# Performance work log

Measured on AMD Instinct MI355X. Metric: run time of the kernel, lower is better.

The kernel has to match this reference:

```python
import jax, jax.numpy as jnp
import numpy as np

N_NODES = 50000


def gcn_conv(x, W, b, src, dst, n):
    """PyG-style GCNConv: symmetric-normalized aggregation over A + I.
    x: [N, Fin], W: [Fin, Fout], b: [Fout], src/dst: [E] int edge endpoints.
    """
    h = x @ W  # [N, Fout]
    # degree with self-loops: deg[i] = 1 + in-degree(i)
    deg = jnp.zeros((n,), dtype=h.dtype).at[dst].add(1.0) + 1.0
    dinv = jax.lax.rsqrt(deg)  # deg^-1/2
    norm_e = dinv[src] * dinv[dst]  # [E]
    # message passing: sum_j norm_ij * h_j  (plus self-loop term deg_i^-1 * h_i)
    agg = jnp.zeros_like(h).at[dst].add(h[src] * norm_e[:, None])
    agg = agg + h * (dinv * dinv)[:, None]
    return agg + b


def setup_inputs() -> dict:
    key = jax.random.key(0)
    ks = jax.random.split(key, 9)
    N, F_in, H, C = N_NODES, 128, 64, 4
    E = 1600000
    node_features = jax.random.normal(ks[0], (N, F_in), dtype=jnp.float32)
    edge_index = jax.random.randint(ks[1], (2, E), 0, N, dtype=jnp.int32)
    s1 = 1.0 / np.sqrt(F_in)
    s2 = 1.0 / np.sqrt(H)
    W1 = jax.random.uniform(ks[2], (F_in, H), jnp.float32, -s1, s1)
    b1 = jax.random.uniform(ks[3], (H,), jnp.float32, -s1, s1)
    W2 = jax.random.uniform(ks[4], (H, H), jnp.float32, -s2, s2)
    b2 = jax.random.uniform(ks[5], (H,), jnp.float32, -s2, s2)
    W3 = jax.random.uniform(ks[6], (H, C), jnp.float32, -s2, s2)
    b3 = jax.random.uniform(ks[7], (C,), jnp.float32, -s2, s2)
    return {"node_features": node_features, "edge_index": edge_index,
            "W1": W1, "b1": b1, "W2": W2, "b2": b2, "W3": W3, "b3": b3}


def reference(node_features, edge_index, W1, b1, W2, b2, W3, b3):
    n = node_features.shape[0]
    src, dst = edge_index[0], edge_index[1]
    out = jax.nn.relu(gcn_conv(node_features, W1, b1, src, dst, n))
    # layer2 applied 7 times with SHARED weights (faithful to the source)
    for _ in range(7):
        out = jax.nn.relu(gcn_conv(out, W2, b2, src, dst, n))
    out = gcn_conv(out, W3, b3, src, dst, n)
    return jax.nn.softmax(out, axis=0)  # softmax over the node dimension (dim=0)
```

## Files before the change

kernel.cpp:

```cpp
#include <hip/hip_runtime.h>
#include <hip/hip_fp16.h>
#include <math.h>
#include <float.h>


#define NPART 8
#define BPP   104


__global__ __launch_bounds__(256) void k_count(const int* __restrict__ dst,
                                               unsigned* __restrict__ deg,
                                               int E, int chunk) {
    int part = blockIdx.x & (NPART - 1);
    int q = blockIdx.x >> 3;
    int lo = part * chunk, hi = lo + chunk;
    for (int e = q * 256 + threadIdx.x; e < E; e += 256 * BPP) {
        int d = dst[e];
        if (d >= lo && d < hi) atomicAdd(&deg[d], 1u);
    }
}

__global__ __launch_bounds__(256) void k_dinv(const unsigned* __restrict__ deg,
                                              float* __restrict__ dinv, int n) {
    int i = blockIdx.x * 256 + threadIdx.x;
    if (i < n) dinv[i] = rsqrtf(1.0f + (float)deg[i]);
}

__global__ __launch_bounds__(256) void k_scan1(const unsigned* __restrict__ deg,
                                               int* __restrict__ row_start,
                                               unsigned* __restrict__ bsum, int n) {
    __shared__ unsigned t[256];
    int i = blockIdx.x * 256 + threadIdx.x;
    unsigned v = (i < n) ? deg[i] : 0u;
    t[threadIdx.x] = v;
    __syncthreads();
    #pragma unroll
    for (int off = 1; off < 256; off <<= 1) {
        unsigned u = (threadIdx.x >= (unsigned)off) ? t[threadIdx.x - off] : 0u;
        __syncthreads();
        t[threadIdx.x] += u;
        __syncthreads();
    }
    if (i < n) row_start[i] = (int)(t[threadIdx.x] - v);
    if (threadIdx.x == 255) bsum[blockIdx.x] = t[255];
}

__global__ __launch_bounds__(256) void k_scan2(unsigned* __restrict__ bsum,
                                               int* __restrict__ row_start,
                                               int nb, int n) {
    __shared__ unsigned t[256];
    unsigned v = (threadIdx.x < (unsigned)nb) ? bsum[threadIdx.x] : 0u;
    t[threadIdx.x] = v;
    __syncthreads();
    #pragma unroll
    for (int off = 1; off < 256; off <<= 1) {
        unsigned u = (threadIdx.x >= (unsigned)off) ? t[threadIdx.x - off] : 0u;
        __syncthreads();
        t[threadIdx.x] += u;
        __syncthreads();
    }
    if (threadIdx.x < (unsigned)nb) bsum[threadIdx.x] = t[threadIdx.x] - v;
    if (threadIdx.x == 255) row_start[n] = (int)t[255];
}

__global__ __launch_bounds__(256) void k_scan3(int* __restrict__ row_start,
                                               const unsigned* __restrict__ bsum, int n) {
    int i = blockIdx.x * 256 + threadIdx.x;
    if (i < n) row_start[i] += (int)bsum[blockIdx.x];
}

__global__ __launch_bounds__(256) void k_fill(const int* __restrict__ src,
                                              const int* __restrict__ dst,
                                              const int* __restrict__ row_start,
                                              unsigned* __restrict__ cursor,
                                              int* __restrict__ csr_src,
                                              int E, int chunk) {
    int part = blockIdx.x & (NPART - 1);
    int q = blockIdx.x >> 3;
    int lo = part * chunk, hi = lo + chunk;
    for (int e = q * 256 + threadIdx.x; e < E; e += 256 * BPP) {
        int d = dst[e];
        if (d >= lo && d < hi) {
            int s = src[e];
            unsigned pos = atomicAdd(&cursor[d], 1u);
            csr_src[row_start[d] + (int)pos] = s;
        }
    }
}


__global__ __launch_bounds__(256) void k_gemm64_f32(const float* __restrict__ x,
                                                    const float* __restrict__ W,
                                                    const float* __restrict__ dinv,
                                                    __half* __restrict__ hs, int n) {
    __shared__ float Wl[128 * 64];
    for (int idx = threadIdx.x; idx < 128 * 64; idx += 256) Wl[idx] = W[idx];
    __syncthreads();
    int wave = threadIdx.x >> 6, lane = threadIdx.x & 63;
    int base = blockIdx.x * 64 + wave * 16;
    for (int it = 0; it < 16; ++it) {
        int i = base + it;
        if (i < n) {
            const float4* xr = (const float4*)(x + (size_t)i * 128);
            float acc = 0.f;
            #pragma unroll
            for (int k4 = 0; k4 < 32; ++k4) {
                float4 v = xr[k4];
                acc += v.x * Wl[(k4 * 4 + 0) * 64 + lane];
                acc += v.y * Wl[(k4 * 4 + 1) * 64 + lane];
                acc += v.z * Wl[(k4 * 4 + 2) * 64 + lane];
                acc += v.w * Wl[(k4 * 4 + 3) * 64 + lane];
            }
            hs[(size_t)i * 64 + lane] = __float2half(acc * dinv[i]);
        }
    }
}


__global__ __launch_bounds__(256) void k_gemm64_f16(const __half* __restrict__ xh,
                                                    const float* __restrict__ W,
                                                    const float* __restrict__ dinv,
                                                    __half* __restrict__ hs, int n) {
    __shared__ float Wl[64 * 64];
    for (int idx = threadIdx.x; idx < 64 * 64; idx += 256) Wl[idx] = W[idx];
    __syncthreads();
    int wave = threadIdx.x >> 6, lane = threadIdx.x & 63;
    int base = blockIdx.x * 64 + wave * 16;
    for (int it = 0; it < 16; ++it) {
        int i = base + it;
        if (i < n) {
            const __half2* xr = (const __half2*)(xh + (size_t)i * 64);
            float acc = 0.f;
            #pragma unroll
            for (int k2 = 0; k2 < 32; ++k2) {
                float2 v = __half22float2(xr[k2]);
                acc += v.x * Wl[(k2 * 2 + 0) * 64 + lane];
                acc += v.y * Wl[(k2 * 2 + 1) * 64 + lane];
            }
            hs[(size_t)i * 64 + lane] = __float2half(acc * dinv[i]);
        }
    }
}

__global__ __launch_bounds__(256) void k_gemm4(const __half* __restrict__ xh,
                                               const float* __restrict__ W,
                                               const float* __restrict__ dinv,
                                               float4* __restrict__ h4, int n) {
    __shared__ float Wl[256];
    for (int idx = threadIdx.x; idx < 256; idx += 256) Wl[idx] = W[idx];
    __syncthreads();
    int i = blockIdx.x * 256 + threadIdx.x;
    if (i >= n) return;
    const __half2* ar = (const __half2*)(xh + (size_t)i * 64);
    float a0 = 0.f, a1 = 0.f, a2 = 0.f, a3 = 0.f;
    #pragma unroll
    for (int k2 = 0; k2 < 32; ++k2) {
        float2 v = __half22float2(ar[k2]);
        int k = k2 * 2;
        a0 += v.x * Wl[k * 4 + 0] + v.y * Wl[(k + 1) * 4 + 0];
        a1 += v.x * Wl[k * 4 + 1] + v.y * Wl[(k + 1) * 4 + 1];
        a2 += v.x * Wl[k * 4 + 2] + v.y * Wl[(k + 1) * 4 + 2];
        a3 += v.x * Wl[k * 4 + 3] + v.y * Wl[(k + 1) * 4 + 3];
    }
    float di = dinv[i];
    h4[i] = make_float4(a0 * di, a1 * di, a2 * di, a3 * di);
}


__global__ __launch_bounds__(256) void k_agg64h(const __half* __restrict__ hs,
                                                const float* __restrict__ dinv,
                                                const int* __restrict__ row_start,
                                                const int* __restrict__ csr_src,
                                                const float* __restrict__ bias,
                                                __half* __restrict__ out, int n) {
    int gw = (int)((blockIdx.x * 256 + threadIdx.x) >> 6);
    int lane = threadIdx.x & 63;
    if (gw >= n) return;
    float acc = __half2float(hs[(size_t)gw * 64 + lane]);
    int s = row_start[gw], e = row_start[gw + 1];
    int slot = s;
    for (; slot + 16 <= e; slot += 16) {
        int idx[16];
        #pragma unroll
        for (int j = 0; j < 16; ++j) idx[j] = csr_src[slot + j];
        float v[16];
        #pragma unroll
        for (int j = 0; j < 16; ++j) v[j] = __half2float(hs[(size_t)idx[j] * 64 + lane]);
        float t0 = ((v[0] + v[1]) + (v[2] + v[3])) + ((v[4] + v[5]) + (v[6] + v[7]));
        float t1 = ((v[8] + v[9]) + (v[10] + v[11])) + ((v[12] + v[13]) + (v[14] + v[15]));
        acc += t0 + t1;
    }
    for (; slot + 4 <= e; slot += 4) {
        int i0 = csr_src[slot + 0], i1 = csr_src[slot + 1];
        int i2 = csr_src[slot + 2], i3 = csr_src[slot + 3];
        float v0 = __half2float(hs[(size_t)i0 * 64 + lane]);
        float v1 = __half2float(hs[(size_t)i1 * 64 + lane]);
        float v2 = __half2float(hs[(size_t)i2 * 64 + lane]);
        float v3 = __half2float(hs[(size_t)i3 * 64 + lane]);
        acc += (v0 + v1) + (v2 + v3);
    }
    for (; slot < e; ++slot)
        acc += __half2float(hs[(size_t)csr_src[slot] * 64 + lane]);
    acc = acc * dinv[gw] + bias[lane];
    out[(size_t)gw * 64 + lane] = __float2half(fmaxf(acc, 0.f));
}


__global__ __launch_bounds__(256) void k_agg4(const float4* __restrict__ h4,
                                              const float* __restrict__ dinv,
                                              const int* __restrict__ row_start,
                                              const int* __restrict__ csr_src,
                                              const float* __restrict__ b3,
                                              float4* __restrict__ z, int n) {
    int i = blockIdx.x * 256 + threadIdx.x;
    if (i >= n) return;
    float4 self = h4[i];
    float a0 = self.x, a1 = self.y, a2 = self.z, a3 = self.w;
    int s = row_start[i], e = row_start[i + 1];
    int slot = s;
    for (; slot + 4 <= e; slot += 4) {
        int s0 = csr_src[slot], s1 = csr_src[slot + 1];
        int s2 = csr_src[slot + 2], s3 = csr_src[slot + 3];
        float4 v0 = h4[s0], v1 = h4[s1], v2 = h4[s2], v3 = h4[s3];
        a0 += v0.x + v1.x + v2.x + v3.x;
        a1 += v0.y + v1.y + v2.y + v3.y;
        a2 += v0.z + v1.z + v2.z + v3.z;
        a3 += v0.w + v1.w + v2.w + v3.w;
    }
    for (; slot < e; ++slot) {
        float4 v = h4[csr_src[slot]];
        a0 += v.x; a1 += v.y; a2 += v.z; a3 += v.w;
    }
    float di = dinv[i];
    z[i] = make_float4(a0 * di + b3[0], a1 * di + b3[1],
                       a2 * di + b3[2], a3 * di + b3[3]);
}


__device__ inline unsigned encf(float f) {
    unsigned u = __float_as_uint(f);
    return (u & 0x80000000u) ? ~u : (u | 0x80000000u);
}
__device__ inline float decf(unsigned e) {
    return (e & 0x80000000u) ? __uint_as_float(e & 0x7FFFFFFFu) : __uint_as_float(~e);
}

__global__ __launch_bounds__(256) void k_max(const float4* __restrict__ z,
                                             unsigned* __restrict__ gmax, int n) {
    float m0 = -FLT_MAX, m1 = -FLT_MAX, m2 = -FLT_MAX, m3 = -FLT_MAX;
    for (int i = blockIdx.x * 256 + threadIdx.x; i < n; i += gridDim.x * 256) {
        float4 v = z[i];
        m0 = fmaxf(m0, v.x); m1 = fmaxf(m1, v.y);
        m2 = fmaxf(m2, v.z); m3 = fmaxf(m3, v.w);
    }
    #pragma unroll
    for (int off = 32; off; off >>= 1) {
        m0 = fmaxf(m0, __shfl_xor(m0, off));
        m1 = fmaxf(m1, __shfl_xor(m1, off));
        m2 = fmaxf(m2, __shfl_xor(m2, off));
        m3 = fmaxf(m3, __shfl_xor(m3, off));
    }
    if ((threadIdx.x & 63) == 0) {
        atomicMax(&gmax[0], encf(m0));
        atomicMax(&gmax[1], encf(m1));
        atomicMax(&gmax[2], encf(m2));
        atomicMax(&gmax[3], encf(m3));
    }
}

__global__ __launch_bounds__(256) void k_exp(const float4* __restrict__ z,
                                             float4* __restrict__ out,
                                             const unsigned* __restrict__ gmax,
                                             float* __restrict__ gsum, int n) {
    float M0 = decf(gmax[0]), M1 = decf(gmax[1]), M2 = decf(gmax[2]), M3 = decf(gmax[3]);
    float s0 = 0.f, s1 = 0.f, s2 = 0.f, s3 = 0.f;
    for (int i = blockIdx.x * 256 + threadIdx.x; i < n; i += gridDim.x * 256) {
        float4 v = z[i];
        float4 e;
        e.x = expf(v.x - M0); e.y = expf(v.y - M1);
        e.z = expf(v.z - M2); e.w = expf(v.w - M3);
        out[i] = e;
        s0 += e.x; s1 += e.y; s2 += e.z; s3 += e.w;
    }
    #pragma unroll
    for (int off = 32; off; off >>= 1) {
        s0 += __shfl_xor(s0, off);
        s1 += __shfl_xor(s1, off);
        s2 += __shfl_xor(s2, off);
        s3 += __shfl_xor(s3, off);
    }
    if ((threadIdx.x & 63) == 0) {
        atomicAdd(&gsum[0], s0);
        atomicAdd(&gsum[1], s1);
        atomicAdd(&gsum[2], s2);
        atomicAdd(&gsum[3], s3);
    }
}

__global__ __launch_bounds__(256) void k_norm(float4* __restrict__ out,
                                              const float* __restrict__ gsum, int n) {
    float r0 = 1.f / gsum[0], r1 = 1.f / gsum[1], r2 = 1.f / gsum[2], r3 = 1.f / gsum[3];
    for (int i = blockIdx.x * 256 + threadIdx.x; i < n; i += gridDim.x * 256) {
        float4 v = out[i];
        v.x *= r0; v.y *= r1; v.z *= r2; v.w *= r3;
        out[i] = v;
    }
}


extern "C" void kernel_launch(void* const* d_in, const int* in_sizes, int n_in,
                              void* d_out, int out_size, void* d_ws, size_t ws_size,
                              hipStream_t stream) {
    const float* x0 = (const float*)d_in[0];
    const int* ei = (const int*)d_in[1];
    const float* W1 = (const float*)d_in[2];
    const float* b1 = (const float*)d_in[3];
    const float* W2 = (const float*)d_in[4];
    const float* b2 = (const float*)d_in[5];
    const float* W3 = (const float*)d_in[6];
    const float* b3 = (const float*)d_in[7];

    const int n = in_sizes[0] / 128;
    const int E = in_sizes[1] / 2;
    const int* src = ei;
    const int* dst = ei + E;
    const int chunk = (n + NPART - 1) / NPART;

    char* ws = (char*)d_ws;
    size_t off = 0;
    auto alloc = [&](size_t bytes) -> void* {
        void* p = (void*)(ws + off);
        off = (off + bytes + 255) & ~(size_t)255;
        return p;
    };

    unsigned* deg    = (unsigned*)alloc((size_t)n * 4);
    unsigned* cursor = (unsigned*)alloc((size_t)n * 4);
    unsigned* gmax   = (unsigned*)alloc(16);
    float*    gsum   = (float*)alloc(16);
    size_t zero_bytes = off;

    float* dinv      = (float*)alloc((size_t)n * 4);
    int*   row_start = (int*)alloc((size_t)(n + 1) * 4);
    unsigned* bsum   = (unsigned*)alloc(1024 * 4);
    int*   csr_src   = (int*)alloc((size_t)E * 4);
    __half* hbuf     = (__half*)alloc((size_t)n * 64 * 2);
    __half* xbuf     = (__half*)alloc((size_t)n * 64 * 2);
    float4* h4buf    = (float4*)alloc((size_t)n * 16);
    float4* zbuf     = (float4*)alloc((size_t)n * 16);

    hipMemsetAsync(deg, 0, zero_bytes, stream);

    const int nbN = (n + 255) / 256;

    k_count<<<NPART * BPP, 256, 0, stream>>>(dst, deg, E, chunk);
    k_dinv<<<nbN, 256, 0, stream>>>(deg, dinv, n);
    k_scan1<<<nbN, 256, 0, stream>>>(deg, row_start, bsum, n);
    k_scan2<<<1, 256, 0, stream>>>(bsum, row_start, nbN, n);
    k_scan3<<<nbN, 256, 0, stream>>>(row_start, bsum, n);
    k_fill<<<NPART * BPP, 256, 0, stream>>>(src, dst, row_start, cursor, csr_src, E, chunk);

    const int nbG = (n + 63) / 64;
    const int nbA = (n * 64 + 255) / 256;

    k_gemm64_f32<<<nbG, 256, 0, stream>>>(x0, W1, dinv, hbuf, n);
    k_agg64h<<<nbA, 256, 0, stream>>>(hbuf, dinv, row_start, csr_src, b1, xbuf, n);

    for (int l = 0; l < 7; ++l) {
        k_gemm64_f16<<<nbG, 256, 0, stream>>>(xbuf, W2, dinv, hbuf, n);
        k_agg64h<<<nbA, 256, 0, stream>>>(hbuf, dinv, row_start, csr_src, b2, xbuf, n);
    }

    k_gemm4<<<nbN, 256, 0, stream>>>(xbuf, W3, dinv, h4buf, n);
    k_agg4<<<nbN, 256, 0, stream>>>(h4buf, dinv, row_start, csr_src, b3, zbuf, n);

    k_max<<<256, 256, 0, stream>>>(zbuf, gmax, n);
    k_exp<<<256, 256, 0, stream>>>(zbuf, (float4*)d_out, gmax, gsum, n);
    k_norm<<<256, 256, 0, stream>>>((float4*)d_out, gsum, n);
}
```

Baseline: 899.4 us.

## Register-block GEMMs over four rows per wave and add nontemporal streaming loads

The dense GEMM kernels now have each wave compute four rows at once. Each shared-memory weight read is reused across four accumulators, and the grid is enlarged so each block handles 16 rows instead of 64. Weight staging into LDS is vectorized with float4. Nontemporal load hints are applied to streamed edge/CSR index reads and GEMM input rows to reduce cache pollution, at the risk of hurting reuse of csr_src across the repeated aggregation layers.

```diff
diff --git a/kernel.cpp b/kernel.cpp
--- a/kernel.cpp
+++ b/kernel.cpp
@@ -6,6 +6,8 @@
 
 #define NPART 8
 #define BPP   104
+
+typedef float f4 __attribute__((ext_vector_type(4)));
 
 
 __global__ __launch_bounds__(256) void k_count(const int* __restrict__ dst,
@@ -15,7 +17,7 @@
     int q = blockIdx.x >> 3;
     int lo = part * chunk, hi = lo + chunk;
     for (int e = q * 256 + threadIdx.x; e < E; e += 256 * BPP) {
-        int d = dst[e];
+        int d = __builtin_nontemporal_load(&dst[e]);
         if (d >= lo && d < hi) atomicAdd(&deg[d], 1u);
     }
 }
@@ -79,9 +81,9 @@
     int q = blockIdx.x >> 3;
     int lo = part * chunk, hi = lo + chunk;
     for (int e = q * 256 + threadIdx.x; e < E; e += 256 * BPP) {
-        int d = dst[e];
+        int d = __builtin_nontemporal_load(&dst[e]);
         if (d >= lo && d < hi) {
-            int s = src[e];
+            int s = __builtin_nontemporal_load(&src[e]);
             unsigned pos = atomicAdd(&cursor[d], 1u);
             csr_src[row_start[d] + (int)pos] = s;
         }
@@ -94,18 +96,47 @@
                                                     const float* __restrict__ dinv,
                                                     __half* __restrict__ hs, int n) {
     __shared__ float Wl[128 * 64];
-    for (int idx = threadIdx.x; idx < 128 * 64; idx += 256) Wl[idx] = W[idx];
+    {
+        const f4* Wv = (const f4*)W;
+        f4* Wlv = (f4*)Wl;
+        for (int idx = threadIdx.x; idx < 128 * 16; idx += 256) Wlv[idx] = Wv[idx];
+    }
     __syncthreads();
     int wave = threadIdx.x >> 6, lane = threadIdx.x & 63;
-    int base = blockIdx.x * 64 + wave * 16;
-    for (int it = 0; it < 16; ++it) {
-        int i = base + it;
-        if (i < n) {
-            const float4* xr = (const float4*)(x + (size_t)i * 128);
+    int i0 = blockIdx.x * 16 + wave * 4;
+    if (i0 >= n) return;
+    if (i0 + 3 < n) {
+        const f4* r0 = (const f4*)(x + (size_t)(i0 + 0) * 128);
+        const f4* r1 = (const f4*)(x + (size_t)(i0 + 1) * 128);
+        const f4* r2 = (const f4*)(x + (size_t)(i0 + 2) * 128);
+        const f4* r3 = (const f4*)(x + (size_t)(i0 + 3) * 128);
+        float a0 = 0.f, a1 = 0.f, a2 = 0.f, a3 = 0.f;
+        #pragma unroll
+        for (int k4 = 0; k4 < 32; ++k4) {
+            f4 v0 = __builtin_nontemporal_load(&r0[k4]);
+            f4 v1 = __builtin_nontemporal_load(&r1[k4]);
+            f4 v2 = __builtin_nontemporal_load(&r2[k4]);
+            f4 v3 = __builtin_nontemporal_load(&r3[k4]);
+            float w0 = Wl[(k4 * 4 + 0) * 64 + lane];
+            float w1 = Wl[(k4 * 4 + 1) * 64 + lane];
+            float w2 = Wl[(k4 * 4 + 2) * 64 + lane];
+            float w3 = Wl[(k4 * 4 + 3) * 64 + lane];
+            a0 += v0.x * w0 + v0.y * w1 + v0.z * w2 + v0.w * w3;
+            a1 += v1.x * w0 + v1.y * w1 + v1.z * w2 + v1.w * w3;
+            a2 += v2.x * w0 + v2.y * w1 + v2.z * w2 + v2.w * w3;
+            a3 += v3.x * w0 + v3.y * w1 + v3.z * w2 + v3.w * w3;
+        }
+        hs[(size_t)(i0 + 0) * 64 + lane] = __float2half(a0 * dinv[i0 + 0]);
+        hs[(size_t)(i0 + 1) * 64 + lane] = __float2half(a1 * dinv[i0 + 1]);
+        hs[(size_t)(i0 + 2) * 64 + lane] = __float2half(a2 * dinv[i0 + 2]);
+        hs[(size_t)(i0 + 3) * 64 + lane] = __float2half(a3 * dinv[i0 + 3]);
+    } else {
+        for (int i = i0; i < n && i < i0 + 4; ++i) {
+            const f4* r = (const f4*)(x + (size_t)i * 128);
             float acc = 0.f;
             #pragma unroll
             for (int k4 = 0; k4 < 32; ++k4) {
-                float4 v = xr[k4];
+                f4 v = r[k4];
                 acc += v.x * Wl[(k4 * 4 + 0) * 64 + lane];
                 acc += v.y * Wl[(k4 * 4 + 1) * 64 + lane];
                 acc += v.z * Wl[(k4 * 4 + 2) * 64 + lane];
@@ -122,18 +153,49 @@
                                                     const float* __restrict__ dinv,
                                                     __half* __restrict__ hs, int n) {
     __shared__ float Wl[64 * 64];
-    for (int idx = threadIdx.x; idx < 64 * 64; idx += 256) Wl[idx] = W[idx];
+    {
+        const f4* Wv = (const f4*)W;
+        f4* Wlv = (f4*)Wl;
+        for (int idx = threadIdx.x; idx < 64 * 16; idx += 256) Wlv[idx] = Wv[idx];
+    }
     __syncthreads();
     int wave = threadIdx.x >> 6, lane = threadIdx.x & 63;
-    int base = blockIdx.x * 64 + wave * 16;
-    for (int it = 0; it < 16; ++it) {
-        int i = base + it;
-        if (i < n) {
-            const __half2* xr = (const __half2*)(xh + (size_t)i * 64);
+    int i0 = blockIdx.x * 16 + wave * 4;
+    if (i0 >= n) return;
+    if (i0 + 3 < n) {
+        const unsigned* r0 = (const unsigned*)(xh + (size_t)(i0 + 0) * 64);
+        const unsigned* r1 = (const unsigned*)(xh + (size_t)(i0 + 1) * 64);
+        const unsigned* r2 = (const unsigned*)(xh + (size_t)(i0 + 2) * 64);
+        const unsigned* r3 = (const unsigned*)(xh + (size_t)(i0 + 3) * 64);
+        float a0 = 0.f, a1 = 0.f, a2 = 0.f, a3 = 0.f;
+        #pragma unroll
+        for (int k2 = 0; k2 < 32; ++k2) {
+            unsigned u0 = __builtin_nontemporal_load(&r0[k2]);
+            unsigned u1 = __builtin_nontemporal_load(&r1[k2]);
+            unsigned u2 = __builtin_nontemporal_load(&r2[k2]);
+            unsigned u3 = __builtin_nontemporal_load(&r3[k2]);
+            float w0 = Wl[(k2 * 2 + 0) * 64 + lane];
+            float w1 = Wl[(k2 * 2 + 1) * 64 + lane];
+            float2 v0 = __half22float2(*(__half2*)&u0);
+            float2 v1 = __half22float2(*(__half2*)&u1);
+            float2 v2 = __half22float2(*(__half2*)&u2);
+            float2 v3 = __half22float2(*(__half2*)&u3);
+            a0 += v0.x * w0 + v0.y * w1;
+            a1 += v1.x * w0 + v1.y * w1;
+            a2 += v2.x * w0 + v2.y * w1;
+            a3 += v3.x * w0 + v3.y * w1;
+        }
+        hs[(size_t)(i0 + 0) * 64 + lane] = __float2half(a0 * dinv[i0 + 0]);
+        hs[(size_t)(i0 + 1) * 64 + lane] = __float2half(a1 * dinv[i0 + 1]);
+        hs[(size_t)(i0 + 2) * 64 + lane] = __float2half(a2 * dinv[i0 + 2]);
+        hs[(size_t)(i0 + 3) * 64 + lane] = __float2half(a3 * dinv[i0 + 3]);
+    } else {
+        for (int i = i0; i < n && i < i0 + 4; ++i) {
+            const __half2* r = (const __half2*)(xh + (size_t)i * 64);
             float acc = 0.f;
             #pragma unroll
             for (int k2 = 0; k2 < 32; ++k2) {
-                float2 v = __half22float2(xr[k2]);
+                float2 v = __half22float2(r[k2]);
                 acc += v.x * Wl[(k2 * 2 + 0) * 64 + lane];
                 acc += v.y * Wl[(k2 * 2 + 1) * 64 + lane];
             }
@@ -182,7 +244,7 @@
     for (; slot + 16 <= e; slot += 16) {
         int idx[16];
         #pragma unroll
-        for (int j = 0; j < 16; ++j) idx[j] = csr_src[slot + j];
+        for (int j = 0; j < 16; ++j) idx[j] = __builtin_nontemporal_load(&csr_src[slot + j]);
         float v[16];
         #pragma unroll
         for (int j = 0; j < 16; ++j) v[j] = __half2float(hs[(size_t)idx[j] * 64 + lane]);
@@ -191,8 +253,10 @@
         acc += t0 + t1;
     }
     for (; slot + 4 <= e; slot += 4) {
-        int i0 = csr_src[slot + 0], i1 = csr_src[slot + 1];
-        int i2 = csr_src[slot + 2], i3 = csr_src[slot + 3];
+        int i0 = __builtin_nontemporal_load(&csr_src[slot + 0]);
+        int i1 = __builtin_nontemporal_load(&csr_src[slot + 1]);
+        int i2 = __builtin_nontemporal_load(&csr_src[slot + 2]);
+        int i3 = __builtin_nontemporal_load(&csr_src[slot + 3]);
         float v0 = __half2float(hs[(size_t)i0 * 64 + lane]);
         float v1 = __half2float(hs[(size_t)i1 * 64 + lane]);
         float v2 = __half2float(hs[(size_t)i2 * 64 + lane]);
@@ -219,8 +283,10 @@
     int s = row_start[i], e = row_start[i + 1];
     int slot = s;
     for (; slot + 4 <= e; slot += 4) {
-        int s0 = csr_src[slot], s1 = csr_src[slot + 1];
-        int s2 = csr_src[slot + 2], s3 = csr_src[slot + 3];
+        int s0 = __builtin_nontemporal_load(&csr_src[slot + 0]);
+        int s1 = __builtin_nontemporal_load(&csr_src[slot + 1]);
+        int s2 = __builtin_nontemporal_load(&csr_src[slot + 2]);
+        int s3 = __builtin_nontemporal_load(&csr_src[slot + 3]);
         float4 v0 = h4[s0], v1 = h4[s1], v2 = h4[s2], v3 = h4[s3];
         a0 += v0.x + v1.x + v2.x + v3.x;
         a1 += v0.y + v1.y + v2.y + v3.y;
@@ -360,7 +426,7 @@
     k_scan3<<<nbN, 256, 0, stream>>>(row_start, bsum, n);
     k_fill<<<NPART * BPP, 256, 0, stream>>>(src, dst, row_start, cursor, csr_src, E, chunk);
 
-    const int nbG = (n + 63) / 64;
+    const int nbG = (n + 15) / 16;
     const int nbA = (n * 64 + 255) / 256;
 
     k_gemm64_f32<<<nbG, 256, 0, stream>>>(x0, W1, dinv, hbuf, n);
```

Result: slower. 992.2 us (+10.3%).
